# Performance work log

Measured on AMD Instinct MI355X. Metric: run time of the kernel, lower is better.

## Reference

```python
import jax, jax.numpy as jnp
import numpy as np

B, L, IN_DIM, OUT_DIM = 4, 2048, 64, 2
D_MODEL, N_LAYERS = 768, 4
D_STATE, EXPAND, D_CONV = 16, 2, 4
D_INNER = EXPAND * D_MODEL          # 1536
DT_RANK = -(-D_MODEL // 16)          # ceil(768/16) = 48
EPS = 1e-5


def rmsnorm(x, w):
    return x * jax.lax.rsqrt(jnp.mean(x * x, axis=-1, keepdims=True) + EPS) * w


def setup_inputs() -> dict:
    key = jax.random.key(0)
    ks = jax.random.split(key, 10)
    s = 0.02
    f = lambda k, shp: jax.random.normal(k, shp, jnp.float32) * s
    return dict(
        x=jax.random.normal(ks[0], (B, L, IN_DIM), jnp.float32),
        W1=f(ks[1], (D_MODEL, IN_DIM)),
        b1=jnp.zeros((D_MODEL,), jnp.float32),
        norm_w=jnp.ones((N_LAYERS, D_MODEL), jnp.float32),
        in_proj_w=f(ks[2], (N_LAYERS, 2 * D_INNER, D_MODEL)),
        conv_w=f(ks[3], (N_LAYERS, D_INNER, D_CONV)),
        conv_b=jnp.zeros((N_LAYERS, D_INNER), jnp.float32),
        x_proj_w=f(ks[4], (N_LAYERS, DT_RANK + 2 * D_STATE, D_INNER)),
        dt_proj_w=f(ks[5], (N_LAYERS, D_INNER, DT_RANK)),
        dt_proj_b=f(ks[6], (N_LAYERS, D_INNER)),
        A_log=jnp.log(jnp.broadcast_to(jnp.arange(1, D_STATE + 1, dtype=jnp.float32), (N_LAYERS, D_INNER, D_STATE))).copy(),
        D=jnp.ones((N_LAYERS, D_INNER), jnp.float32),
        out_proj_w=f(ks[7], (N_LAYERS, D_MODEL, D_INNER)),
        normf_w=jnp.ones((D_MODEL,), jnp.float32),
        W2=f(ks[8], (OUT_DIM, D_MODEL)),
        b2=jnp.zeros((OUT_DIM,), jnp.float32),
    )


def _block(h, p):
    # One Mamba residual block (mamba-minimal): h + out_proj(ssm(conv(in_proj(norm(h)))))
    norm_w, in_w, cw, cb, xp_w, dt_w, dt_b, A_log, Dp, out_w = p
    xn = rmsnorm(h, norm_w)
    xr = xn @ in_w.T                                  # [B,L,2*d_inner]
    xs, res = jnp.split(xr, 2, axis=-1)
    # causal depthwise conv1d, kernel D_CONV, left pad D_CONV-1
    xc = jax.lax.conv_general_dilated(
        xs.transpose(0, 2, 1), cw[:, None, :], (1,), [(D_CONV - 1, 0)],
        feature_group_count=D_INNER, dimension_numbers=('NCH', 'OIH', 'NCH'))
    xc = jax.nn.silu((xc + cb[None, :, None]).transpose(0, 2, 1))  # [B,L,d_inner]
    # selective SSM
    A = -jnp.exp(A_log)                               # [d_inner, n]
    dbl = xc @ xp_w.T                                 # [B,L,dt_rank+2n]
    dr = dbl[..., :DT_RANK]
    Bm = dbl[..., DT_RANK:DT_RANK + D_STATE]          # [B,L,n]
    Cm = dbl[..., DT_RANK + D_STATE:]                 # [B,L,n]
    delta = jax.nn.softplus(dr @ dt_w.T + dt_b)       # [B,L,d_inner]

    def step(s, t):
        d_t, B_t, C_t, u_t = t                        # [B,d_in],[B,n],[B,n],[B,d_in]
        dA = jnp.exp(d_t[..., None] * A)              # [B,d_in,n]
        s = dA * s + (d_t * u_t)[..., None] * B_t[:, None, :]
        y = jnp.einsum('bdn,bn->bd', s, C_t)
        return s, y

    init = jnp.zeros((h.shape[0], D_INNER, D_STATE), h.dtype)
    ts = (delta.transpose(1, 0, 2), Bm.transpose(1, 0, 2),
          Cm.transpose(1, 0, 2), xc.transpose(1, 0, 2))
    _, ys = jax.lax.scan(step, init, ts)
    y = ys.transpose(1, 0, 2) + xc * Dp               # [B,L,d_inner]
    y = y * jax.nn.silu(res)
    return h + y @ out_w.T


def _forward(x, W1, b1, norm_w, in_proj_w, conv_w, conv_b, x_proj_w,
             dt_proj_w, dt_proj_b, A_log, D, out_proj_w, normf_w, W2, b2):
    h = x @ W1.T + b1                                 # [B,L,d_model]
    params = (norm_w, in_proj_w, conv_w, conv_b, x_proj_w, dt_proj_w,
              dt_proj_b, A_log, D, out_proj_w)
    h, _ = jax.lax.scan(lambda c, p: (_block(c, p), None), h, params)
    h = rmsnorm(h, normf_w)
    logits = h @ W2.T + b2                            # [B,L,out_dim]
    probs = jax.nn.softmax(logits, axis=1)            # Softmax(dim=1) over L
    return probs.reshape(-1)                          # x.flatten()


def reference(x, W1, b1, norm_w, in_proj_w, conv_w, conv_b, x_proj_w,
              dt_proj_w, dt_proj_b, A_log, D, out_proj_w, normf_w, W2, b2):
    return _forward(x, W1, b1, norm_w, in_proj_w, conv_w, conv_b, x_proj_w,
                    dt_proj_w, dt_proj_b, A_log, D, out_proj_w, normf_w, W2, b2)
```

## Files before the change

kernel.cpp:

```cpp
#include <hip/hip_runtime.h>

typedef __bf16 bf16_t;
typedef bf16_t bf16x8 __attribute__((ext_vector_type(8)));
typedef float f32x4 __attribute__((ext_vector_type(4)));

#define DEV_INLINE __device__ __forceinline__

#define BB 4
#define LL 2048
#define ROWS 8192
#define DMODEL 768
#define DINNER 1536
#define DIN2 3072
#define DTRANK 48
#define DSTATE 16

DEV_INLINE void glds16(const void* g, void* l) {
    __builtin_amdgcn_global_load_lds(
        (const __attribute__((address_space(1))) void*)(unsigned long long)g,
        (__attribute__((address_space(3))) void*)(unsigned int)(unsigned long long)l,
        16, 0, 0);
}

DEV_INLINE float bf2f(bf16_t v) { return (float)v; }
DEV_INLINE bf16_t f2bf(float v) { return (bf16_t)v; }

struct Ptrs { const void* p[16]; };

__device__ __constant__ const int g_off[16] = {
    0, 524288, 573440, 574208, 577280, 10014464, 10039040, 10045184,
    10536704, 10831616, 10837760, 10936064, 10942208, 15660800, 15661568, 15663104
};
__device__ __constant__ const int g_sz[16] = {
    524288, 49152, 768, 3072, 9437184, 24576, 6144, 491520,
    294912, 6144, 98304, 6144, 4718592, 768, 1536, 2
};
#define CONV_ELEMS 15663112

__global__ __launch_bounds__(256) void convert_inputs(Ptrs P, bf16_t* __restrict__ dst,
                                                      float* __restrict__ Aa)
{
    int i = blockIdx.x * 256 + threadIdx.x;
    if (i >= CONV_ELEMS) return;
    bool isbf = (*(const unsigned*)P.p[3] == 0x3F803F80u);
    int seg = -1; int rel = 0;
#pragma unroll
    for (int s = 0; s < 16; ++s) {
        int r = i - g_off[s];
        if (r >= 0 && r < g_sz[s]) { seg = s; rel = r; }
    }
    if (seg < 0) return;
    const void* sp = P.p[seg];
    float fv = isbf ? bf2f(((const bf16_t*)sp)[rel]) : ((const float*)sp)[rel];
    dst[i] = f2bf(fv);
    if (seg == 10) Aa[rel] = -__expf(fv);
}

__global__ __launch_bounds__(256) void gemm_bt128(
    const bf16_t* __restrict__ A, int lda,
    const bf16_t* __restrict__ W, int ldw,
    void* __restrict__ Cv, int ldc, int K,
    const bf16_t* __restrict__ bias, int epi)
{
    __shared__ bf16_t sA[128 * 32];
    __shared__ bf16_t sW[128 * 32];
    const int t = threadIdx.x;
    const int wv = t >> 6, lane = t & 63;
    const int qk = lane >> 4, lr = lane & 15;
    const int m0 = blockIdx.x * 128, n0 = blockIdx.y * 128;
    const int wm = (wv >> 1) * 64, wn = (wv & 1) * 64;

    f32x4 acc[4][4];
#pragma unroll
    for (int i = 0; i < 4; ++i)
#pragma unroll
        for (int j = 0; j < 4; ++j) acc[i][j] = (f32x4){0.f, 0.f, 0.f, 0.f};

    for (int k0 = 0; k0 < K; k0 += 32) {
        __syncthreads();
#pragma unroll
        for (int j = 0; j < 2; ++j) {
            int chunk = (wv * 2 + j) * 64 + lane;
            int row = chunk >> 2;
            int c = chunk & 3;
            int g = c ^ ((row >> 1) & 3);
            const char* srcA = (const char*)(A + (size_t)(m0 + row) * lda + k0) + g * 16;
            const char* srcW = (const char*)(W + (size_t)(n0 + row) * ldw + k0) + g * 16;
            glds16(srcA, (char*)sA + (wv * 2 + j) * 1024);
            glds16(srcW, (char*)sW + (wv * 2 + j) * 1024);
        }
        __syncthreads();

        bf16x8 af[4], wf[4];
#pragma unroll
        for (int i = 0; i < 4; ++i) {
            int row = wm + i * 16 + lr;
            int cc = qk ^ ((row >> 1) & 3);
            af[i] = *(const bf16x8*)((const char*)sA + row * 64 + cc * 16);
        }
#pragma unroll
        for (int j = 0; j < 4; ++j) {
            int row = wn + j * 16 + lr;
            int cc = qk ^ ((row >> 1) & 3);
            wf[j] = *(const bf16x8*)((const char*)sW + row * 64 + cc * 16);
        }
#pragma unroll
        for (int i = 0; i < 4; ++i)
#pragma unroll
            for (int j = 0; j < 4; ++j)
                acc[i][j] = __builtin_amdgcn_mfma_f32_16x16x32_bf16(af[i], wf[j], acc[i][j], 0, 0, 0);
    }

    float* Cf = (float*)Cv;
    bf16_t* Cb = (bf16_t*)Cv;
#pragma unroll
    for (int i = 0; i < 4; ++i) {
        int row = m0 + wm + i * 16 + qk * 4;
#pragma unroll
        for (int j = 0; j < 4; ++j) {
            int col = n0 + wn + j * 16 + lr;
#pragma unroll
            for (int r = 0; r < 4; ++r) {
                size_t idx = (size_t)(row + r) * ldc + col;
                float v = acc[i][j][r];
                if (epi == 1) v += bf2f(bias[col]);
                if (epi == 2) v += Cf[idx];
                if (epi == 3) Cb[idx] = f2bf(v);
                else Cf[idx] = v;
            }
        }
    }
}

__global__ __launch_bounds__(256) void gemm_xproj(
    const bf16_t* __restrict__ A,
    const bf16_t* __restrict__ W,
    float* __restrict__ Cp)
{
    __shared__ bf16_t sA[64 * 32];
    __shared__ bf16_t sW[80 * 32];
    const int t = threadIdx.x;
    const int wv = t >> 6, lane = t & 63;
    const int qk = lane >> 4, lr = lane & 15;
    const int m0 = blockIdx.x * 64;
    const int z  = blockIdx.y;
    const int wm = wv * 16;

    f32x4 acc[5];
#pragma unroll
    for (int j = 0; j < 5; ++j) acc[j] = (f32x4){0.f, 0.f, 0.f, 0.f};

    const int kbeg = z * (DINNER / 2), kend = kbeg + DINNER / 2;
    for (int k0 = kbeg; k0 < kend; k0 += 32) {
        __syncthreads();
        {
            int chunk = wv * 64 + lane;
            int row = chunk >> 2;
            int c = chunk & 3;
            int g = c ^ ((row >> 1) & 3);
            const char* srcA = (const char*)(A + (size_t)(m0 + row) * DINNER + k0) + g * 16;
            glds16(srcA, (char*)sA + wv * 1024);
        }
        for (int issue = wv; issue < 5; issue += 4) {
            int chunk = issue * 64 + lane;
            int row = chunk >> 2;
            int c = chunk & 3;
            int g = c ^ ((row >> 1) & 3);
            const char* srcW = (const char*)(W + (size_t)row * DINNER + k0) + g * 16;
            glds16(srcW, (char*)sW + issue * 1024);
        }
        __syncthreads();

        int rowa = wm + lr;
        int cca = qk ^ ((rowa >> 1) & 3);
        bf16x8 af = *(const bf16x8*)((const char*)sA + rowa * 64 + cca * 16);
#pragma unroll
        for (int j = 0; j < 5; ++j) {
            int roww = j * 16 + lr;
            int ccw = qk ^ ((roww >> 1) & 3);
            bf16x8 wf = *(const bf16x8*)((const char*)sW + roww * 64 + ccw * 16);
            acc[j] = __builtin_amdgcn_mfma_f32_16x16x32_bf16(af, wf, acc[j], 0, 0, 0);
        }
    }

    float* Co = Cp + (size_t)z * ROWS * 80;
    int row = m0 + wm + qk * 4;
#pragma unroll
    for (int j = 0; j < 5; ++j) {
        int col = j * 16 + lr;
#pragma unroll
        for (int r = 0; r < 4; ++r)
            Co[(size_t)(row + r) * 80 + col] = acc[j][r];
    }
}

__global__ __launch_bounds__(256) void xproj_combine(
    const float* __restrict__ Cp, bf16_t* __restrict__ dbl)
{
    int i = blockIdx.x * 256 + threadIdx.x;
    if (i < ROWS * 80)
        dbl[i] = f2bf(Cp[i] + Cp[(size_t)ROWS * 80 + i]);
}

__global__ __launch_bounds__(256) void gemm_dtproj(
    const bf16_t* __restrict__ A,
    const bf16_t* __restrict__ W,
    const bf16_t* __restrict__ bias,
    bf16_t* __restrict__ C)
{
    __shared__ bf16_t sA[128 * 32];
    __shared__ bf16_t sW[128 * 32];
    const int t = threadIdx.x;
    const int wv = t >> 6, lane = t & 63;
    const int qk = lane >> 4, lr = lane & 15;
    const int m0 = blockIdx.x * 128, n0 = blockIdx.y * 128;
    const int wm = (wv >> 1) * 64, wn = (wv & 1) * 64;

    f32x4 acc[4][4];
#pragma unroll
    for (int i = 0; i < 4; ++i)
#pragma unroll
        for (int j = 0; j < 4; ++j) acc[i][j] = (f32x4){0.f, 0.f, 0.f, 0.f};

    for (int k0 = 0; k0 < 64; k0 += 32) {
        __syncthreads();
#pragma unroll
        for (int j = 0; j < 2; ++j) {
            int chunk = j * 256 + t;
            int row = chunk >> 2;
            int c = chunk & 3;
            int g = c ^ ((row >> 1) & 3);
            int gb = k0 * 2 + g * 16;
            uint4 va = {0u, 0u, 0u, 0u}, vw = {0u, 0u, 0u, 0u};
            if (gb < 96) {
                va = *(const uint4*)((const char*)(A + (size_t)(m0 + row) * 80) + gb);
                vw = *(const uint4*)((const char*)(W + (size_t)(n0 + row) * DTRANK) + gb);
            }
            *(uint4*)((char*)sA + chunk * 16) = va;
            *(uint4*)((char*)sW + chunk * 16) = vw;
        }
        __syncthreads();

        bf16x8 af[4], wf[4];
#pragma unroll
        for (int i = 0; i < 4; ++i) {
            int row = wm + i * 16 + lr;
            int cc = qk ^ ((row >> 1) & 3);
            af[i] = *(const bf16x8*)((const char*)sA + row * 64 + cc * 16);
        }
#pragma unroll
        for (int j = 0; j < 4; ++j) {
            int row = wn + j * 16 + lr;
            int cc = qk ^ ((row >> 1) & 3);
            wf[j] = *(const bf16x8*)((const char*)sW + row * 64 + cc * 16);
        }
#pragma unroll
        for (int i = 0; i < 4; ++i)
#pragma unroll
            for (int j = 0; j < 4; ++j)
                acc[i][j] = __builtin_amdgcn_mfma_f32_16x16x32_bf16(af[i], wf[j], acc[i][j], 0, 0, 0);
    }

#pragma unroll
    for (int i = 0; i < 4; ++i) {
        int row = m0 + wm + i * 16 + qk * 4;
#pragma unroll
        for (int j = 0; j < 4; ++j) {
            int col = n0 + wn + j * 16 + lr;
            float bv = bf2f(bias[col]);
#pragma unroll
            for (int r = 0; r < 4; ++r) {
                float v = acc[i][j][r] + bv;
                v = (v > 30.f) ? v : log1pf(__expf(v));
                C[(size_t)(row + r) * DINNER + col] = f2bf(v);
            }
        }
    }
}

__global__ __launch_bounds__(256) void rmsnorm_kernel(
    const float* __restrict__ h, const bf16_t* __restrict__ w, bf16_t* __restrict__ out)
{
    int row = blockIdx.x;
    int tid = threadIdx.x;
    const float* hr = h + (size_t)row * DMODEL;
    float ss = 0.f;
    for (int k = tid; k < DMODEL; k += 256) { float v = hr[k]; ss += v * v; }
#pragma unroll
    for (int off = 32; off > 0; off >>= 1) ss += __shfl_down(ss, off);
    __shared__ float red[4];
    if ((tid & 63) == 0) red[tid >> 6] = ss;
    __syncthreads();
    float tot = red[0] + red[1] + red[2] + red[3];
    float scale = rsqrtf(tot / (float)DMODEL + 1e-5f);
    for (int k = tid; k < DMODEL; k += 256)
        out[(size_t)row * DMODEL + k] = f2bf(hr[k] * scale * bf2f(w[k]));
}

__global__ __launch_bounds__(256) void conv_silu_kernel(
    const bf16_t* __restrict__ xr, const bf16_t* __restrict__ cw,
    const bf16_t* __restrict__ cb, bf16_t* __restrict__ xc)
{
    int idx = blockIdx.x * 256 + threadIdx.x;
    int row = idx / 192;
    int d8 = (idx - row * 192) * 8;
    int l = row & (LL - 1);

    bf16x8 cbv = *(const bf16x8*)(cb + d8);
    bf16x8 cw4[4];
#pragma unroll
    for (int m = 0; m < 4; ++m) cw4[m] = *(const bf16x8*)(cw + d8 * 4 + m * 8);

    float acc[8];
#pragma unroll
    for (int k = 0; k < 8; ++k) acc[k] = bf2f(cbv[k]);

#pragma unroll
    for (int j = 0; j < 4; ++j) {
        if (l - 3 + j >= 0) {
            bf16x8 xv = *(const bf16x8*)(xr + (size_t)(row - 3 + j) * DIN2 + d8);
#pragma unroll
            for (int k = 0; k < 8; ++k) {
                int wi = k * 4 + j;
                acc[k] += bf2f(xv[k]) * bf2f(cw4[wi >> 3][wi & 7]);
            }
        }
    }
    bf16x8 ov;
#pragma unroll
    for (int k = 0; k < 8; ++k) {
        float s = acc[k] / (1.f + __expf(-acc[k]));
        ov[k] = f2bf(s);
    }
    *(bf16x8*)(xc + (size_t)row * DINNER + d8) = ov;
}

__global__ __launch_bounds__(256) void scan_p1(
    const bf16_t* __restrict__ delta, const bf16_t* __restrict__ xc,
    const bf16_t* __restrict__ dbl, const float* __restrict__ Aa_l,
    float* __restrict__ carryDt, float* __restrict__ carryE,
    int nchunk, int clen)
{
    int d = blockIdx.x * 256 + threadIdx.x;
    int b = blockIdx.y / nchunk, c = blockIdx.y - b * nchunk;
    float Aa[DSTATE];
#pragma unroll
    for (int n = 0; n < DSTATE; ++n) Aa[n] = Aa_l[d * DSTATE + n];
    float Aa0 = Aa[0];
    bool geo = true;
#pragma unroll
    for (int n = 1; n < DSTATE; ++n)
        geo = geo && (fabsf(Aa[n] - (float)(n + 1) * Aa0) <= 0.02f * (float)(n + 1) * fabsf(Aa0));

    float s[DSTATE];
#pragma unroll
    for (int n = 0; n < DSTATE; ++n) s[n] = 0.f;
    float dtsum = 0.f;
    int row0 = b * LL + c * clen;

    if (geo) {
        for (int tt = 0; tt < clen; ++tt) {
            size_t row = row0 + tt;
            float dt = bf2f(delta[row * DINNER + d]);
            float du = dt * bf2f(xc[row * DINNER + d]);
            bf16x8 B0 = *(const bf16x8*)(dbl + row * 80 + 48);
            bf16x8 B1 = *(const bf16x8*)(dbl + row * 80 + 56);
            float r = __expf(dt * Aa0);
            float dA = 1.f;
#pragma unroll
            for (int n = 0; n < DSTATE; ++n) {
                float bv = (n < 8) ? bf2f(B0[n & 7]) : bf2f(B1[n & 7]);
                dA *= r;
                s[n] = dA * s[n] + du * bv;
            }
            dtsum += dt;
        }
    } else {
        for (int tt = 0; tt < clen; ++tt) {
            size_t row = row0 + tt;
            float dt = bf2f(delta[row * DINNER + d]);
            float du = dt * bf2f(xc[row * DINNER + d]);
            bf16x8 B0 = *(const bf16x8*)(dbl + row * 80 + 48);
            bf16x8 B1 = *(const bf16x8*)(dbl + row * 80 + 56);
#pragma unroll
            for (int n = 0; n < DSTATE; ++n) {
                float bv = (n < 8) ? bf2f(B0[n & 7]) : bf2f(B1[n & 7]);
                float dA = __expf(dt * Aa[n]);
                s[n] = dA * s[n] + du * bv;
            }
            dtsum += dt;
        }
    }

    size_t eb = ((size_t)(b * nchunk + c) * DINNER + d) * DSTATE;
#pragma unroll
    for (int n = 0; n < DSTATE; ++n) carryE[eb + n] = s[n];
    carryDt[(size_t)(b * nchunk + c) * DINNER + d] = dtsum;
}

__global__ __launch_bounds__(256) void scan_p2(
    const float* __restrict__ carryDt, float* __restrict__ carryE,
    const float* __restrict__ Aa_l, int nchunk)
{
    int idx = blockIdx.x * 256 + threadIdx.x;
    int n = idx & 15;
    int bd = idx >> 4;
    int b = bd / DINNER, d = bd - b * DINNER;
    float Aa = Aa_l[d * DSTATE + n];
    float act = 0.f;
    for (int c = 0; c < nchunk; ++c) {
        size_t rowbase = (size_t)(b * nchunk + c) * DINNER + d;
        float P = __expf(carryDt[rowbase] * Aa);
        size_t ep = rowbase * DSTATE + n;
        float E = carryE[ep];
        carryE[ep] = act;
        act = P * act + E;
    }
}

__global__ __launch_bounds__(256) void scan_p3(
    const bf16_t* __restrict__ delta, const bf16_t* __restrict__ xc,
    const bf16_t* __restrict__ dbl, const float* __restrict__ Aa_l,
    const float* __restrict__ carryInit, const bf16_t* __restrict__ xr,
    const bf16_t* __restrict__ Dp_l, bf16_t* __restrict__ y,
    int nchunk, int clen)
{
    int d = blockIdx.x * 256 + threadIdx.x;
    int b = blockIdx.y / nchunk, c = blockIdx.y - b * nchunk;
    float Aa[DSTATE];
#pragma unroll
    for (int n = 0; n < DSTATE; ++n) Aa[n] = Aa_l[d * DSTATE + n];
    float Aa0 = Aa[0];
    bool geo = true;
#pragma unroll
    for (int n = 1; n < DSTATE; ++n)
        geo = geo && (fabsf(Aa[n] - (float)(n + 1) * Aa0) <= 0.02f * (float)(n + 1) * fabsf(Aa0));

    float s[DSTATE];
    size_t eb = ((size_t)(b * nchunk + c) * DINNER + d) * DSTATE;
#pragma unroll
    for (int n = 0; n < DSTATE; ++n) s[n] = carryInit[eb + n];
    float Dv = bf2f(Dp_l[d]);
    int row0 = b * LL + c * clen;

    if (geo) {
        for (int tt = 0; tt < clen; ++tt) {
            size_t row = row0 + tt;
            float dt = bf2f(delta[row * DINNER + d]);
            float u = bf2f(xc[row * DINNER + d]);
            float du = dt * u;
            bf16x8 B0 = *(const bf16x8*)(dbl + row * 80 + 48);
            bf16x8 B1 = *(const bf16x8*)(dbl + row * 80 + 56);
            bf16x8 C0 = *(const bf16x8*)(dbl + row * 80 + 64);
            bf16x8 C1 = *(const bf16x8*)(dbl + row * 80 + 72);
            float r = __expf(dt * Aa0);
            float dA = 1.f;
            float yv = 0.f;
#pragma unroll
            for (int n = 0; n < DSTATE; ++n) {
                float bv = (n < 8) ? bf2f(B0[n & 7]) : bf2f(B1[n & 7]);
                float cvv = (n < 8) ? bf2f(C0[n & 7]) : bf2f(C1[n & 7]);
                dA *= r;
                s[n] = dA * s[n] + du * bv;
                yv += s[n] * cvv;
            }
            float res = bf2f(xr[row * DIN2 + DINNER + d]);
            float sr = res / (1.f + __expf(-res));
            y[row * DINNER + d] = f2bf((yv + u * Dv) * sr);
        }
    } else {
        for (int tt = 0; tt < clen; ++tt) {
            size_t row = row0 + tt;
            float dt = bf2f(delta[row * DINNER + d]);
            float u = bf2f(xc[row * DINNER + d]);
            float du = dt * u;
            bf16x8 B0 = *(const bf16x8*)(dbl + row * 80 + 48);
            bf16x8 B1 = *(const bf16x8*)(dbl + row * 80 + 56);
            bf16x8 C0 = *(const bf16x8*)(dbl + row * 80 + 64);
            bf16x8 C1 = *(const bf16x8*)(dbl + row * 80 + 72);
            float yv = 0.f;
#pragma unroll
            for (int n = 0; n < DSTATE; ++n) {
                float bv = (n < 8) ? bf2f(B0[n & 7]) : bf2f(B1[n & 7]);
                float cvv = (n < 8) ? bf2f(C0[n & 7]) : bf2f(C1[n & 7]);
                float dA = __expf(dt * Aa[n]);
                s[n] = dA * s[n] + du * bv;
                yv += s[n] * cvv;
            }
            float res = bf2f(xr[row * DIN2 + DINNER + d]);
            float sr = res / (1.f + __expf(-res));
            y[row * DINNER + d] = f2bf((yv + u * Dv) * sr);
        }
    }
}

__global__ __launch_bounds__(256) void head_kernel(
    const bf16_t* __restrict__ hn, const bf16_t* __restrict__ W2,
    const bf16_t* __restrict__ b2, float* __restrict__ logits)
{
    int wv = threadIdx.x >> 6, lane = threadIdx.x & 63;
    int row = blockIdx.x * 4 + wv;
    const bf16_t* hr = hn + (size_t)row * DMODEL;
    float a0 = 0.f, a1 = 0.f;
    for (int k = lane; k < DMODEL; k += 64) {
        float x = bf2f(hr[k]);
        a0 += x * bf2f(W2[k]);
        a1 += x * bf2f(W2[DMODEL + k]);
    }
#pragma unroll
    for (int off = 32; off > 0; off >>= 1) {
        a0 += __shfl_down(a0, off);
        a1 += __shfl_down(a1, off);
    }
    if (lane == 0) {
        logits[(size_t)row * 2 + 0] = a0 + bf2f(b2[0]);
        logits[(size_t)row * 2 + 1] = a1 + bf2f(b2[1]);
    }
}

__global__ __launch_bounds__(256) void softmax_kernel(
    const float* __restrict__ logits, void* __restrict__ outv,
    const void* __restrict__ norm_raw)
{
    bool isbf = (*(const unsigned*)norm_raw == 0x3F803F80u);
    int b = blockIdx.x >> 1, o = blockIdx.x & 1;
    int tid = threadIdx.x;
    __shared__ float red[256];
    float mx = -1e30f;
    for (int l = tid; l < LL; l += 256)
        mx = fmaxf(mx, logits[(size_t)(b * LL + l) * 2 + o]);
    red[tid] = mx; __syncthreads();
    for (int s2 = 128; s2 > 0; s2 >>= 1) {
        if (tid < s2) red[tid] = fmaxf(red[tid], red[tid + s2]);
        __syncthreads();
    }
    mx = red[0];
    __syncthreads();
    float sum = 0.f;
    for (int l = tid; l < LL; l += 256)
        sum += __expf(logits[(size_t)(b * LL + l) * 2 + o] - mx);
    red[tid] = sum; __syncthreads();
    for (int s2 = 128; s2 > 0; s2 >>= 1) {
        if (tid < s2) red[tid] += red[tid + s2];
        __syncthreads();
    }
    float inv = 1.f / red[0];
    for (int l = tid; l < LL; l += 256) {
        float e = __expf(logits[(size_t)(b * LL + l) * 2 + o] - mx);
        float p = e * inv;
        if (!(p == p)) p = 999.0f;
        size_t oi = (size_t)(b * LL + l) * 2 + o;
        if (isbf) ((bf16_t*)outv)[oi] = f2bf(p);
        else      ((float*)outv)[oi] = p;
    }
}

extern "C" void kernel_launch(void* const* d_in, const int* in_sizes, int n_in,
                              void* d_out, int out_size, void* d_ws, size_t ws_size,
                              hipStream_t stream)
{
    char* ws = (char*)d_ws;
    bf16_t* cv     = (bf16_t*)(ws + 0ull);
    float*  Aaf    = (float*) (ws + 31326464ull);
    float*  h      = (float*) (ws + 31719680ull);
    bf16_t* xr     = (bf16_t*)(ws + 56885504ull);
    bf16_t* xny    = (bf16_t*)(ws + 107217152ull);
    bf16_t* xc     = (bf16_t*)(ws + 132382976ull);
    bf16_t* delta  = (bf16_t*)(ws + 157548800ull);
    bf16_t* dbl    = (bf16_t*)(ws + 182714624ull);
    float*  logits = (float*) (ws + 184025344ull);
    const size_t fixed_end = 184090880ull;
    float* dblP = (float*)(ws + 157548800ull);

    int nchunk = 16;
    if (ws_size >= fixed_end + 417792ull * 64) nchunk = 64;
    else if (ws_size >= fixed_end + 417792ull * 32) nchunk = 32;
    int clen = LL / nchunk;
    float* carryE  = (float*)(ws + fixed_end);
    float* carryDt = (float*)(ws + fixed_end + 393216ull * nchunk);

    const bf16_t* x      = cv + 0;
    const bf16_t* W1     = cv + 524288;
    const bf16_t* b1     = cv + 573440;
    const bf16_t* norm_w = cv + 574208;
    const bf16_t* in_w   = cv + 577280;
    const bf16_t* conv_w = cv + 10014464;
    const bf16_t* conv_b = cv + 10039040;
    const bf16_t* xp_w   = cv + 10045184;
    const bf16_t* dt_w   = cv + 10536704;
    const bf16_t* dt_b   = cv + 10831616;
    const bf16_t* Dp     = cv + 10936064;
    const bf16_t* out_w  = cv + 10942208;
    const bf16_t* normf_w= cv + 15660800;
    const bf16_t* W2     = cv + 15661568;
    const bf16_t* b2     = cv + 15663104;

    dim3 blk(256);

    Ptrs P;
    for (int i = 0; i < 16; ++i) P.p[i] = d_in[i];
    convert_inputs<<<(CONV_ELEMS + 255) / 256, blk, 0, stream>>>(P, cv, Aaf);

    bf16_t* xn = xny;
    bf16_t* y  = xny;

    gemm_bt128<<<dim3(64, 6), blk, 0, stream>>>(x, 64, W1, 64, (void*)h, DMODEL, 64, b1, 1);

    for (int l = 0; l < 4; ++l) {
        const bf16_t* in_w_l  = in_w  + (size_t)l * DIN2 * DMODEL;
        const bf16_t* xp_w_l  = xp_w  + (size_t)l * 80 * DINNER;
        const bf16_t* dt_w_l  = dt_w  + (size_t)l * DINNER * DTRANK;
        const bf16_t* out_w_l = out_w + (size_t)l * DMODEL * DINNER;
        const float*  Aa_l    = Aaf   + (size_t)l * DINNER * DSTATE;

        rmsnorm_kernel<<<ROWS, blk, 0, stream>>>(h, norm_w + l * DMODEL, xn);
        gemm_bt128<<<dim3(64, 24), blk, 0, stream>>>(xn, DMODEL, in_w_l, DMODEL,
                                                     (void*)xr, DIN2, DMODEL, nullptr, 3);
        conv_silu_kernel<<<ROWS * 192 / 256, blk, 0, stream>>>(xr, conv_w + l * DINNER * 4,
                                                               conv_b + l * DINNER, xc);
        gemm_xproj<<<dim3(128, 2), blk, 0, stream>>>(xc, xp_w_l, dblP);
        xproj_combine<<<ROWS * 80 / 256, blk, 0, stream>>>(dblP, dbl);
        gemm_dtproj<<<dim3(64, 12), blk, 0, stream>>>(dbl, dt_w_l, dt_b + l * DINNER, delta);
        scan_p1<<<dim3(6, BB * nchunk), blk, 0, stream>>>(delta, xc, dbl, Aa_l,
                                                          carryDt, carryE, nchunk, clen);
        scan_p2<<<BB * DINNER * DSTATE / 256, blk, 0, stream>>>(carryDt, carryE, Aa_l, nchunk);
        scan_p3<<<dim3(6, BB * nchunk), blk, 0, stream>>>(delta, xc, dbl, Aa_l, carryE,
                                                          xr, Dp + l * DINNER, y, nchunk, clen);
        gemm_bt128<<<dim3(64, 6), blk, 0, stream>>>(y, DINNER, out_w_l, DINNER,
                                                    (void*)h, DMODEL, DINNER, nullptr, 2);
    }

    rmsnorm_kernel<<<ROWS, blk, 0, stream>>>(h, normf_w, xn);
    head_kernel<<<ROWS / 4, blk, 0, stream>>>(xn, W2, b2, logits);
    softmax_kernel<<<8, blk, 0, stream>>>(logits, (void*)d_out, d_in[3]);
}
```

Baseline: 1.426 ms.

## Deepen GEMM K-tile to 64 and add smaller-M out_proj kernel

The bf16 GEMMs now stage 64-wide K slices per iteration with an 8-way XOR swizzle, which halves the number of barrier-separated load rounds. The dt_proj GEMM loads its whole K in a single pass. A dedicated out_proj kernel uses 64-row M tiles, doubling the grid from 384 to 768 blocks so more CUs have work, and accumulates directly into h. The cost is doubled LDS per block, which may lower occupancy.

```diff
diff --git a/kernel.cpp b/kernel.cpp
--- a/kernel.cpp
+++ b/kernel.cpp
@@ -62,8 +62,8 @@
     void* __restrict__ Cv, int ldc, int K,
     const bf16_t* __restrict__ bias, int epi)
 {
-    __shared__ bf16_t sA[128 * 32];
-    __shared__ bf16_t sW[128 * 32];
+    __shared__ bf16_t sA[128 * 64];
+    __shared__ bf16_t sW[128 * 64];
     const int t = threadIdx.x;
     const int wv = t >> 6, lane = t & 63;
     const int qk = lane >> 4, lr = lane & 15;
@@ -76,39 +76,42 @@
 #pragma unroll
         for (int j = 0; j < 4; ++j) acc[i][j] = (f32x4){0.f, 0.f, 0.f, 0.f};
 
-    for (int k0 = 0; k0 < K; k0 += 32) {
+    for (int k0 = 0; k0 < K; k0 += 64) {
         __syncthreads();
 #pragma unroll
-        for (int j = 0; j < 2; ++j) {
-            int chunk = (wv * 2 + j) * 64 + lane;
-            int row = chunk >> 2;
-            int c = chunk & 3;
-            int g = c ^ ((row >> 1) & 3);
+        for (int j = 0; j < 4; ++j) {
+            int ci = (wv * 4 + j) * 64 + lane;
+            int row = ci >> 3;
+            int c = ci & 7;
+            int g = c ^ (row & 7);
             const char* srcA = (const char*)(A + (size_t)(m0 + row) * lda + k0) + g * 16;
             const char* srcW = (const char*)(W + (size_t)(n0 + row) * ldw + k0) + g * 16;
-            glds16(srcA, (char*)sA + (wv * 2 + j) * 1024);
-            glds16(srcW, (char*)sW + (wv * 2 + j) * 1024);
+            glds16(srcA, (char*)sA + ci * 16);
+            glds16(srcW, (char*)sW + ci * 16);
         }
         __syncthreads();
 
-        bf16x8 af[4], wf[4];
-#pragma unroll
-        for (int i = 0; i < 4; ++i) {
-            int row = wm + i * 16 + lr;
-            int cc = qk ^ ((row >> 1) & 3);
-            af[i] = *(const bf16x8*)((const char*)sA + row * 64 + cc * 16);
-        }
-#pragma unroll
-        for (int j = 0; j < 4; ++j) {
-            int row = wn + j * 16 + lr;
-            int cc = qk ^ ((row >> 1) & 3);
-            wf[j] = *(const bf16x8*)((const char*)sW + row * 64 + cc * 16);
-        }
-#pragma unroll
-        for (int i = 0; i < 4; ++i)
-#pragma unroll
-            for (int j = 0; j < 4; ++j)
-                acc[i][j] = __builtin_amdgcn_mfma_f32_16x16x32_bf16(af[i], wf[j], acc[i][j], 0, 0, 0);
+#pragma unroll
+        for (int h = 0; h < 2; ++h) {
+            bf16x8 af[4], wf[4];
+#pragma unroll
+            for (int i = 0; i < 4; ++i) {
+                int row = wm + i * 16 + lr;
+                int cc = (h * 4 + qk) ^ (row & 7);
+                af[i] = *(const bf16x8*)((const char*)sA + row * 128 + cc * 16);
+            }
+#pragma unroll
+            for (int j = 0; j < 4; ++j) {
+                int row = wn + j * 16 + lr;
+                int cc = (h * 4 + qk) ^ (row & 7);
+                wf[j] = *(const bf16x8*)((const char*)sW + row * 128 + cc * 16);
+            }
+#pragma unroll
+            for (int i = 0; i < 4; ++i)
+#pragma unroll
+                for (int j = 0; j < 4; ++j)
+                    acc[i][j] = __builtin_amdgcn_mfma_f32_16x16x32_bf16(af[i], wf[j], acc[i][j], 0, 0, 0);
+        }
     }
 
     float* Cf = (float*)Cv;
@@ -127,6 +130,83 @@
                 if (epi == 2) v += Cf[idx];
                 if (epi == 3) Cb[idx] = f2bf(v);
                 else Cf[idx] = v;
+            }
+        }
+    }
+}
+
+__global__ __launch_bounds__(256) void gemm_outproj(
+    const bf16_t* __restrict__ A,
+    const bf16_t* __restrict__ W,
+    float* __restrict__ Cf)
+{
+    __shared__ bf16_t sA[64 * 64];
+    __shared__ bf16_t sW[128 * 64];
+    const int t = threadIdx.x;
+    const int wv = t >> 6, lane = t & 63;
+    const int qk = lane >> 4, lr = lane & 15;
+    const int m0 = blockIdx.x * 64, n0 = blockIdx.y * 128;
+    const int wm = (wv >> 1) * 32, wn = (wv & 1) * 64;
+
+    f32x4 acc[2][4];
+#pragma unroll
+    for (int i = 0; i < 2; ++i)
+#pragma unroll
+        for (int j = 0; j < 4; ++j) acc[i][j] = (f32x4){0.f, 0.f, 0.f, 0.f};
+
+    for (int k0 = 0; k0 < DINNER; k0 += 64) {
+        __syncthreads();
+#pragma unroll
+        for (int j = 0; j < 2; ++j) {
+            int ci = (wv * 2 + j) * 64 + lane;
+            int row = ci >> 3;
+            int g = (ci & 7) ^ (row & 7);
+            const char* srcA = (const char*)(A + (size_t)(m0 + row) * DINNER + k0) + g * 16;
+            glds16(srcA, (char*)sA + ci * 16);
+        }
+#pragma unroll
+        for (int j = 0; j < 4; ++j) {
+            int ci = (wv * 4 + j) * 64 + lane;
+            int row = ci >> 3;
+            int g = (ci & 7) ^ (row & 7);
+            const char* srcW = (const char*)(W + (size_t)(n0 + row) * DINNER + k0) + g * 16;
+            glds16(srcW, (char*)sW + ci * 16);
+        }
+        __syncthreads();
+
+#pragma unroll
+        for (int h = 0; h < 2; ++h) {
+            bf16x8 af[2], wf[4];
+#pragma unroll
+            for (int i = 0; i < 2; ++i) {
+                int row = wm + i * 16 + lr;
+                int cc = (h * 4 + qk) ^ (row & 7);
+                af[i] = *(const bf16x8*)((const char*)sA + row * 128 + cc * 16);
+            }
+#pragma unroll
+            for (int j = 0; j < 4; ++j) {
+                int row = wn + j * 16 + lr;
+                int cc = (h * 4 + qk) ^ (row & 7);
+                wf[j] = *(const bf16x8*)((const char*)sW + row * 128 + cc * 16);
+            }
+#pragma unroll
+            for (int i = 0; i < 2; ++i)
+#pragma unroll
+                for (int j = 0; j < 4; ++j)
+                    acc[i][j] = __builtin_amdgcn_mfma_f32_16x16x32_bf16(af[i], wf[j], acc[i][j], 0, 0, 0);
+        }
+    }
+
+#pragma unroll
+    for (int i = 0; i < 2; ++i) {
+        int row = m0 + wm + i * 16 + qk * 4;
+#pragma unroll
+        for (int j = 0; j < 4; ++j) {
+            int col = n0 + wn + j * 16 + lr;
+#pragma unroll
+            for (int r = 0; r < 4; ++r) {
+                size_t idx = (size_t)(row + r) * DMODEL + col;
+                Cf[idx] += acc[i][j][r];
             }
         }
     }
@@ -208,51 +288,50 @@
     const bf16_t* __restrict__ bias,
     bf16_t* __restrict__ C)
 {
-    __shared__ bf16_t sA[128 * 32];
-    __shared__ bf16_t sW[128 * 32];
+    __shared__ bf16_t sA[128 * 64];
+    __shared__ bf16_t sW[128 * 64];
     const int t = threadIdx.x;
     const int wv = t >> 6, lane = t & 63;
     const int qk = lane >> 4, lr = lane & 15;
     const int m0 = blockIdx.x * 128, n0 = blockIdx.y * 128;
     const int wm = (wv >> 1) * 64, wn = (wv & 1) * 64;
 
+#pragma unroll
+    for (int j = 0; j < 4; ++j) {
+        int ci = j * 256 + t;
+        int row = ci >> 3;
+        int g = (ci & 7) ^ (row & 7);
+        int gb = g * 16;
+        uint4 va = {0u, 0u, 0u, 0u}, vw = {0u, 0u, 0u, 0u};
+        if (gb < 96) {
+            va = *(const uint4*)((const char*)(A + (size_t)(m0 + row) * 80) + gb);
+            vw = *(const uint4*)((const char*)(W + (size_t)(n0 + row) * DTRANK) + gb);
+        }
+        *(uint4*)((char*)sA + ci * 16) = va;
+        *(uint4*)((char*)sW + ci * 16) = vw;
+    }
+    __syncthreads();
+
     f32x4 acc[4][4];
 #pragma unroll
     for (int i = 0; i < 4; ++i)
 #pragma unroll
         for (int j = 0; j < 4; ++j) acc[i][j] = (f32x4){0.f, 0.f, 0.f, 0.f};
 
-    for (int k0 = 0; k0 < 64; k0 += 32) {
-        __syncthreads();
-#pragma unroll
-        for (int j = 0; j < 2; ++j) {
-            int chunk = j * 256 + t;
-            int row = chunk >> 2;
-            int c = chunk & 3;
-            int g = c ^ ((row >> 1) & 3);
-            int gb = k0 * 2 + g * 16;
-            uint4 va = {0u, 0u, 0u, 0u}, vw = {0u, 0u, 0u, 0u};
-            if (gb < 96) {
-                va = *(const uint4*)((const char*)(A + (size_t)(m0 + row) * 80) + gb);
-                vw = *(const uint4*)((const char*)(W + (size_t)(n0 + row) * DTRANK) + gb);
-            }
-            *(uint4*)((char*)sA + chunk * 16) = va;
-            *(uint4*)((char*)sW + chunk * 16) = vw;
-        }
-        __syncthreads();
-
+#pragma unroll
+    for (int h = 0; h < 2; ++h) {
         bf16x8 af[4], wf[4];
 #pragma unroll
         for (int i = 0; i < 4; ++i) {
             int row = wm + i * 16 + lr;
-            int cc = qk ^ ((row >> 1) & 3);
-            af[i] = *(const bf16x8*)((const char*)sA + row * 64 + cc * 16);
+            int cc = (h * 4 + qk) ^ (row & 7);
+            af[i] = *(const bf16x8*)((const char*)sA + row * 128 + cc * 16);
         }
 #pragma unroll
         for (int j = 0; j < 4; ++j) {
             int row = wn + j * 16 + lr;
-            int cc = qk ^ ((row >> 1) & 3);
-            wf[j] = *(const bf16x8*)((const char*)sW + row * 64 + cc * 16);
+            int cc = (h * 4 + qk) ^ (row & 7);
+            wf[j] = *(const bf16x8*)((const char*)sW + row * 128 + cc * 16);
         }
 #pragma unroll
         for (int i = 0; i < 4; ++i)
@@ -626,8 +705,7 @@
         scan_p2<<<BB * DINNER * DSTATE / 256, blk, 0, stream>>>(carryDt, carryE, Aa_l, nchunk);
         scan_p3<<<dim3(6, BB * nchunk), blk, 0, stream>>>(delta, xc, dbl, Aa_l, carryE,
                                                           xr, Dp + l * DINNER, y, nchunk, clen);
-        gemm_bt128<<<dim3(64, 6), blk, 0, stream>>>(y, DINNER, out_w_l, DINNER,
-                                                    (void*)h, DMODEL, DINNER, nullptr, 2);
+        gemm_outproj<<<dim3(128, 6), blk, 0, stream>>>(y, out_w_l, h);
     }
 
     rmsnorm_kernel<<<ROWS, blk, 0, stream>>>(h, normf_w, xn);
```

Result: faster. 1.296 ms (-9.1%).
